# Kernel optimization log

Hardware: AMD Instinct MI355X
Metric: run time of the kernel (lower is better)

Reference implementation:

```python
import jax, jax.numpy as jnp
import numpy as np

N_ATOMS = 10000
N_STRUCT = 100
N_PSEUDO = 4
N_SPECIES = 4
NMAX = 8
LMAX = 3
HIDDEN = 256
Q = NMAX * N_PSEUDO            # 32 radial*pseudo channels per l
N_FEAT = (LMAX + 1) * Q * Q    # 4096


def setup_inputs() -> dict:
    key = jax.random.key(0)
    ks = jax.random.split(key, 12)
    inp = {}
    for l in range(LMAX + 1):
        inp[f"c{l}"] = jax.random.normal(ks[l], (N_ATOMS, 2 * l + 1, Q), dtype=jnp.float32)
    inp["species_idx"] = jax.random.randint(ks[4], (N_ATOMS,), 0, N_SPECIES, dtype=jnp.int32)
    inp["structure_ids"] = jnp.sort(jax.random.randint(ks[5], (N_ATOMS,), 0, N_STRUCT, dtype=jnp.int32))
    inp["comb_W"] = jax.random.normal(ks[6], (N_PSEUDO, N_SPECIES), dtype=jnp.float32) / np.sqrt(N_SPECIES).astype(np.float32)
    inp["W0"] = jax.random.normal(ks[7], (N_PSEUDO, N_FEAT, HIDDEN), dtype=jnp.float32) / np.sqrt(N_FEAT).astype(np.float32)
    inp["W1"] = jax.random.normal(ks[8], (N_PSEUDO, HIDDEN, HIDDEN), dtype=jnp.float32) / np.sqrt(HIDDEN).astype(np.float32)
    inp["W2"] = jax.random.normal(ks[9], (N_PSEUDO, HIDDEN, 1), dtype=jnp.float32) / np.sqrt(HIDDEN).astype(np.float32)
    return inp


def _power_spectrum(cs):
    # Per-atom outer-product contraction over m, per angular order l.
    feats = []
    for l, c in enumerate(cs):  # c: [A, 2l+1, Q]
        cg = np.float32(1.0 / np.sqrt(2 * l + 1))
        ps = cg * jnp.einsum('amq,amr->aqr', c, c)  # [A, Q, Q]
        feats.append(ps.reshape(c.shape[0], -1))
    return jnp.concatenate(feats, axis=-1)  # [A, N_FEAT]


def reference(c0, c1, c2, c3, species_idx, structure_ids, comb_W, W0, W1, W2):
    features = _power_spectrum([c0, c1, c2, c3])  # [A, F]
    # species-gathered pseudo-species weights: one_hot(a_i) @ combination_matrix
    one_hot = jax.nn.one_hot(species_idx, N_SPECIES, dtype=features.dtype)  # [A, S]
    pw = one_hot @ comb_W.T  # [A, P]
    # embedded_features = features[:, :, None] * pw[:, None, :]
    emb = features[:, None, :] * pw[:, :, None]  # [A, P, F]
    # distinct no-bias MLP per pseudo species (SiLU activations)
    h = jax.nn.silu(jnp.einsum('apf,pfh->aph', emb, W0))
    h = jax.nn.silu(jnp.einsum('aph,phg->apg', h, W1))
    atomic = jnp.einsum('apg,pgo->apo', h, W2)[..., 0].sum(axis=1)  # [A]
    # scatter-sum atomic energies into per-structure totals (index_add_)
    energies = jax.ops.segment_sum(atomic, structure_ids, num_segments=N_STRUCT)
    return energies.reshape(-1, 1)
```

## Files before the change

### kernel.cpp

```cpp
#include <hip/hip_runtime.h>
#include <hip/hip_bf16.h>
#include <cstdint>
#include <cstddef>

#define N_ATOMS 10000
#define NSTRUCT 100
#define NP 4
#define NS 4
#define NF2 2560
#define HID 256
#define APAD 10240

#define PB_FEAT  2500
#define PB_W0    (PB_FEAT + 2560)
#define PB_W1    (PB_W0 + 256)
#define PB_ZERO  (PB_W1 + 300)
#define PB_TOTAL (PB_ZERO + 1)

typedef __attribute__((ext_vector_type(8))) _Float16 f16x8;
typedef __attribute__((ext_vector_type(8))) ushort u16x8;
typedef __attribute__((ext_vector_type(4))) float f32x4;

__device__ __forceinline__ float silu(float x) {
  return x / (1.f + __expf(-x));
}
__device__ __forceinline__ ushort f2h(float x) {
  _Float16 h = (_Float16)x;
  return *reinterpret_cast<ushort*>(&h);
}
__device__ __forceinline__ void cdec(int c, int& q, int& b) {
  if (c < 32)      { q = c >> 2; b = c & 3; }
  else if (c < 56) { int x = c - 32; int j = (x * 171) >> 9; q = 8 + j; b = 1 + (x - j * 3); }
  else if (c < 72) { int x = c - 56; q = 16 + (x >> 1); b = 2 + (x & 1); }
  else             { q = 24 + (c - 72); b = 3; }
}

typedef __attribute__((address_space(3))) uint32_t lds_u32;
typedef const __attribute__((address_space(1))) uint32_t glb_u32;
__device__ __forceinline__ void glds16(const ushort* g, ushort* l) {
  __builtin_amdgcn_global_load_lds((glb_u32*)g, (lds_u32*)l, 16, 0, 0);
}

__global__ __launch_bounds__(256) void prep_kernel(
    const float* __restrict__ c0, const float* __restrict__ c1,
    const float* __restrict__ c2, const float* __restrict__ c3,
    const float* __restrict__ W0, const float* __restrict__ W1,
    ushort* __restrict__ fh, ushort* __restrict__ W0t,
    ushort* __restrict__ W1t, float* __restrict__ out) {
  __shared__ float shbuf[2048];
  int b = blockIdx.x;
  int tid = threadIdx.x;

  if (b < PB_FEAT) {
    int wv = tid >> 6, lane = tid & 63;
    int a = b * 4 + wv;
    float* cs = shbuf + wv * 512;
    for (int i = 0; i < 8; ++i) {
      int e = lane + i * 64;
      float v;
      if (e < 32)       v = c0[a * 32  + e];
      else if (e < 128) v = c1[a * 96  + (e - 32)];
      else if (e < 288) v = c2[a * 160 + (e - 128)];
      else              v = c3[a * 224 + (e - 288)];
      cs[e] = v;
    }
    __syncthreads();
    const float cg[4]  = {1.0f, 0.5773502691896258f, 0.4472135954999579f, 0.3779644730092272f};
    const int  off[4]  = {0, 32, 128, 288};
    const int  nm[4]   = {1, 3, 5, 7};
#pragma unroll
    for (int t = 0; t < 5; ++t) {
      int cc = lane + t * 64;
      int l = cc / 80, c = cc - l * 80;
      int q, bb; cdec(c, q, bb);
      int rb = bb * 8;
      const float* base = cs + off[l];
      float s[8] = {0.f, 0.f, 0.f, 0.f, 0.f, 0.f, 0.f, 0.f};
      for (int m = 0; m < nm[l]; ++m) {
        float bq = base[m * 32 + q];
        float4 v0 = *reinterpret_cast<const float4*>(&base[m * 32 + rb]);
        float4 v1 = *reinterpret_cast<const float4*>(&base[m * 32 + rb + 4]);
        s[0] += bq * v0.x; s[1] += bq * v0.y; s[2] += bq * v0.z; s[3] += bq * v0.w;
        s[4] += bq * v1.x; s[5] += bq * v1.y; s[6] += bq * v1.z; s[7] += bq * v1.w;
      }
      u16x8 o;
#pragma unroll
      for (int u = 0; u < 8; ++u) o[u] = f2h(s[u] * cg[l]);
      *reinterpret_cast<u16x8*>(&fh[(size_t)a * NF2 + cc * 8]) = o;
    }
  } else if (b < PB_W0) {
    int idx = b - PB_FEAT;
    int nx = idx & 7;
    int rest = idx >> 3;
    int ky = rest % 80, p = rest / 80;
    int kt = ky * 32, nt = nx * 32;
    int lx = tid & 31, ly = tid >> 5;
    float (*t)[33] = (float(*)[33])shbuf;
    const float* src = W0 + (size_t)p * 4096 * HID;
#pragma unroll
    for (int i = 0; i < 4; ++i) {
      int kf = kt + ly + i * 8;
      int l = kf / 640, w = kf - l * 640;
      int c = w >> 3, s = w & 7;
      int q, bb; cdec(c, q, bb);
      int r = bb * 8 + s;
      float v = 0.f;
      if (r >= q) {
        v = src[(size_t)(l * 1024 + q * 32 + r) * HID + nt + lx];
        if (r > q) v += src[(size_t)(l * 1024 + r * 32 + q) * HID + nt + lx];
      }
      t[ly + i * 8][lx] = v;
    }
    __syncthreads();
    ushort* dst = W0t + (size_t)p * HID * NF2;
#pragma unroll
    for (int i = 0; i < 4; ++i)
      dst[(size_t)(nt + ly + i * 8) * NF2 + kt + lx] = f2h(t[lx][ly + i * 8]);
  } else if (b < PB_W1) {
    int idx = b - PB_W0;
    int nx = idx & 7, ky = (idx >> 3) & 7, p = idx >> 6;
    int kt = ky * 32, nt = nx * 32;
    int lx = tid & 31, ly = tid >> 5;
    float (*t)[33] = (float(*)[33])shbuf;
    const float* src = W1 + (size_t)p * HID * HID;
#pragma unroll
    for (int i = 0; i < 4; ++i)
      t[ly + i * 8][lx] = src[(size_t)(kt + ly + i * 8) * HID + nt + lx];
    __syncthreads();
    ushort* dst = W1t + (size_t)p * HID * HID;
#pragma unroll
    for (int i = 0; i < 4; ++i)
      dst[(size_t)(nt + ly + i * 8) * HID + kt + lx] = f2h(t[lx][ly + i * 8]);
  } else if (b < PB_ZERO) {
    int idx = b - PB_W1;
    size_t e = (size_t)idx * 2048 + tid * 8;
    u16x8 z = (u16x8){0, 0, 0, 0, 0, 0, 0, 0};
    *reinterpret_cast<u16x8*>(&fh[(size_t)N_ATOMS * NF2 + e]) = z;
  } else {
    if (tid < NSTRUCT) out[tid] = 0.f;
  }
}

__global__ __launch_bounds__(256) void gemm0_mfma(
    const ushort* __restrict__ fh, const ushort* __restrict__ W0t,
    const float* __restrict__ combW, const int* __restrict__ species,
    ushort* __restrict__ h0f) {
  __shared__ ushort As[64 * 64];
  __shared__ ushort Bs[64 * 64];
  int tid = threadIdx.x;
  int linear = blockIdx.y * 8 + blockIdx.x;
  int xc = linear & 7, sq = linear >> 3;
  int bm = ((sq >> 3) * 8 + xc) * 128;
  int bn = (sq & 7) * 128;
  int wid = tid >> 6, lane = tid & 63;
  int wm = (wid >> 1) * 64, wn = (wid & 1) * 64;
  int mh = wid >> 1, nh = wid & 1;

  int pr = tid >> 3, pc = tid & 7;
  int lg = pc ^ (pr & 7);
  int mhalf = lg >> 2, kc = lg & 3;
  const ushort* gaA1 = fh  + ((size_t)(bm + pr + 64 * mhalf) * NF2 + kc * 8);
  const ushort* gaA2 = gaA1 + (size_t)32 * NF2;
  const ushort* gaB1 = W0t + ((size_t)(bn + pr + 64 * mhalf) * NF2 + kc * 8);
  const ushort* gaB2 = gaB1 + (size_t)32 * NF2;
  ushort* lA = As + tid * 8;
  ushort* lB = Bs + tid * 8;

  f32x4 acc[4][4];
#pragma unroll
  for (int i = 0; i < 4; ++i)
#pragma unroll
    for (int j = 0; j < 4; ++j) acc[i][j] = (f32x4){0.f, 0.f, 0.f, 0.f};

  int mrow = lane & 15;
  int h7 = mrow & 7;
  int qv = lane >> 4;
  int pcA = ((mh << 2) | qv) ^ h7;
  int pcB = ((nh << 2) | qv) ^ h7;

  for (int k0 = 0; k0 < NF2; k0 += 32) {
    glds16(gaA1 + k0, lA);
    glds16(gaA2 + k0, lA + 2048);
    glds16(gaB1 + k0, lB);
    glds16(gaB2 + k0, lB + 2048);
    __syncthreads();

    f16x8 af[4], bf[4];
#pragma unroll
    for (int i = 0; i < 4; ++i) {
      af[i] = *reinterpret_cast<const f16x8*>(&As[(i * 16 + mrow) * 64 + pcA * 8]);
      bf[i] = *reinterpret_cast<const f16x8*>(&Bs[(i * 16 + mrow) * 64 + pcB * 8]);
    }
#pragma unroll
    for (int i = 0; i < 4; ++i)
#pragma unroll
      for (int j = 0; j < 4; ++j)
        acc[i][j] = __builtin_amdgcn_mfma_f32_16x16x32_f16(af[i], bf[j], acc[i][j], 0, 0, 0);
    __syncthreads();
  }

  int p = bn >> 8;
  int col = lane & 15, rbase = (lane >> 4) * 4;
#pragma unroll
  for (int i = 0; i < 4; ++i) {
#pragma unroll
    for (int r = 0; r < 4; ++r) {
      int m = bm + wm + i * 16 + rbase + r;
      bool live = (m < N_ATOMS);
      float pw = live ? combW[p * NS + species[m]] : 0.f;
#pragma unroll
      for (int j = 0; j < 4; ++j) {
        int n = bn + wn + j * 16 + col;
        float v = live ? silu(pw * acc[i][j][r]) : 0.f;
        h0f[(size_t)m * 1024 + n] = f2h(v);
      }
    }
  }
}

__global__ __launch_bounds__(256) void mlp1_mfma(
    const ushort* __restrict__ h0f, const ushort* __restrict__ W1t,
    const float* __restrict__ W2, const int* __restrict__ sid,
    float* __restrict__ out) {
  __shared__ ushort As[64 * 256];
  __shared__ float sout[NSTRUCT];
  int tid = threadIdx.x;
  int linear = blockIdx.x;
  int xc = linear & 7, s = linear >> 3;
  int p = s & 3, t = s >> 2;
  int bm = ((t >> 1) * 8 + xc) * 128 + (t & 1) * 64;
  int wid = tid >> 6, lane = tid & 63;
  int wn = wid * 64;

  if (tid < NSTRUCT) sout[tid] = 0.f;

  int mrow = lane & 15;
  int qv = lane >> 4;
  int h7 = mrow & 7;

#pragma unroll
  for (int s8 = 0; s8 < 8; ++s8) {
    int d = s8 * 256 + tid;
    int r = d >> 5, pcs = d & 31;
    int lc = pcs ^ (r & 7);
    glds16(h0f + (size_t)(bm + r) * 1024 + p * 256 + lc * 8, As + d * 8);
  }

  const ushort* wb = W1t + (size_t)p * HID * HID;
  f16x8 breg[4][8];
#pragma unroll
  for (int j = 0; j < 4; ++j) {
    const ushort* row = wb + (size_t)(wn + j * 16 + mrow) * 256 + qv * 8;
#pragma unroll
    for (int ki = 0; ki < 8; ++ki)
      breg[j][ki] = *reinterpret_cast<const f16x8*>(row + ki * 32);
  }

  __syncthreads();

  f32x4 acc[4][4];
#pragma unroll
  for (int i = 0; i < 4; ++i)
#pragma unroll
    for (int j = 0; j < 4; ++j) acc[i][j] = (f32x4){0.f, 0.f, 0.f, 0.f};

#pragma unroll
  for (int ki = 0; ki < 8; ++ki) {
    f16x8 af[4];
#pragma unroll
    for (int i = 0; i < 4; ++i) {
      int row = i * 16 + mrow;
      int pc2 = (ki * 4 + qv) ^ h7;
      af[i] = *reinterpret_cast<const f16x8*>(&As[row * 256 + pc2 * 8]);
    }
#pragma unroll
    for (int i = 0; i < 4; ++i)
#pragma unroll
      for (int j = 0; j < 4; ++j)
        acc[i][j] = __builtin_amdgcn_mfma_f32_16x16x32_f16(af[i], breg[j][ki], acc[i][j], 0, 0, 0);
  }

  int col = lane & 15, quad = lane >> 4;
  float w2j[4];
#pragma unroll
  for (int j = 0; j < 4; ++j) w2j[j] = W2[p * 256 + wn + j * 16 + col];
#pragma unroll
  for (int i = 0; i < 4; ++i) {
#pragma unroll
    for (int r = 0; r < 4; ++r) {
      float v = silu(acc[i][0][r]) * w2j[0] + silu(acc[i][1][r]) * w2j[1]
              + silu(acc[i][2][r]) * w2j[2] + silu(acc[i][3][r]) * w2j[3];
      v += __shfl_xor(v, 1, 64);
      v += __shfl_xor(v, 2, 64);
      v += __shfl_xor(v, 4, 64);
      v += __shfl_xor(v, 8, 64);
      if (col == 0) {
        int m = bm + i * 16 + quad * 4 + r;
        if (m < N_ATOMS) atomicAdd(&sout[sid[m]], v);
      }
    }
  }
  __syncthreads();
  if (tid < NSTRUCT) {
    float v = sout[tid];
    if (v != 0.f) atomicAdd(&out[tid], v);
  }
}

extern "C" void kernel_launch(void* const* d_in, const int* in_sizes, int n_in,
                              void* d_out, int out_size, void* d_ws, size_t ws_size,
                              hipStream_t stream) {
  const float* c0      = (const float*)d_in[0];
  const float* c1      = (const float*)d_in[1];
  const float* c2      = (const float*)d_in[2];
  const float* c3      = (const float*)d_in[3];
  const int*   species = (const int*)d_in[4];
  const int*   sid     = (const int*)d_in[5];
  const float* combW   = (const float*)d_in[6];
  const float* W0      = (const float*)d_in[7];
  const float* W1      = (const float*)d_in[8];
  const float* W2      = (const float*)d_in[9];
  float*       out     = (float*)d_out;

  ushort* fh  = (ushort*)d_ws;
  ushort* W0t = fh  + (size_t)APAD * NF2;
  ushort* W1t = W0t + (size_t)NP * HID * NF2;
  ushort* h0f = W1t + (size_t)NP * HID * HID;

  prep_kernel<<<PB_TOTAL, 256, 0, stream>>>(c0, c1, c2, c3, W0, W1,
                                            fh, W0t, W1t, out);

  dim3 g2(8, APAD / 128);
  gemm0_mfma<<<g2, 256, 0, stream>>>(fh, W0t, combW, species, h0f);

  mlp1_mfma<<<640, 256, 0, stream>>>(h0f, W1t, W2, sid, out);
}
```

Measured before the change: 206.3 us.

## Fuse first-layer GEMM with second-layer MLP to eliminate h0 round trip

Merges the W0 GEMM kernel and the W1/W2 MLP kernel into one kernel. Each block computes a 64-row by 256-hidden tile for one pseudo species, writes the SiLU output into shared memory, then runs the W1 GEMM and W2 reduction from there. This removes the global write and read of the fp16 h0 buffer and one kernel launch. In exchange the first GEMM now uses 64x256 tiles with 4x more B traffic per A row, and W1 fragments are loaded inside the k loop rather than preloaded into registers.

```diff
diff --git a/kernel.cpp b/kernel.cpp
--- a/kernel.cpp
+++ b/kernel.cpp
@@ -141,89 +141,15 @@
   }
 }
 
-__global__ __launch_bounds__(256) void gemm0_mfma(
+__global__ __launch_bounds__(256) void gemm_fused(
     const ushort* __restrict__ fh, const ushort* __restrict__ W0t,
+    const ushort* __restrict__ W1t, const float* __restrict__ W2,
     const float* __restrict__ combW, const int* __restrict__ species,
-    ushort* __restrict__ h0f) {
-  __shared__ ushort As[64 * 64];
-  __shared__ ushort Bs[64 * 64];
-  int tid = threadIdx.x;
-  int linear = blockIdx.y * 8 + blockIdx.x;
-  int xc = linear & 7, sq = linear >> 3;
-  int bm = ((sq >> 3) * 8 + xc) * 128;
-  int bn = (sq & 7) * 128;
-  int wid = tid >> 6, lane = tid & 63;
-  int wm = (wid >> 1) * 64, wn = (wid & 1) * 64;
-  int mh = wid >> 1, nh = wid & 1;
-
-  int pr = tid >> 3, pc = tid & 7;
-  int lg = pc ^ (pr & 7);
-  int mhalf = lg >> 2, kc = lg & 3;
-  const ushort* gaA1 = fh  + ((size_t)(bm + pr + 64 * mhalf) * NF2 + kc * 8);
-  const ushort* gaA2 = gaA1 + (size_t)32 * NF2;
-  const ushort* gaB1 = W0t + ((size_t)(bn + pr + 64 * mhalf) * NF2 + kc * 8);
-  const ushort* gaB2 = gaB1 + (size_t)32 * NF2;
-  ushort* lA = As + tid * 8;
-  ushort* lB = Bs + tid * 8;
-
-  f32x4 acc[4][4];
-#pragma unroll
-  for (int i = 0; i < 4; ++i)
-#pragma unroll
-    for (int j = 0; j < 4; ++j) acc[i][j] = (f32x4){0.f, 0.f, 0.f, 0.f};
-
-  int mrow = lane & 15;
-  int h7 = mrow & 7;
-  int qv = lane >> 4;
-  int pcA = ((mh << 2) | qv) ^ h7;
-  int pcB = ((nh << 2) | qv) ^ h7;
-
-  for (int k0 = 0; k0 < NF2; k0 += 32) {
-    glds16(gaA1 + k0, lA);
-    glds16(gaA2 + k0, lA + 2048);
-    glds16(gaB1 + k0, lB);
-    glds16(gaB2 + k0, lB + 2048);
-    __syncthreads();
-
-    f16x8 af[4], bf[4];
-#pragma unroll
-    for (int i = 0; i < 4; ++i) {
-      af[i] = *reinterpret_cast<const f16x8*>(&As[(i * 16 + mrow) * 64 + pcA * 8]);
-      bf[i] = *reinterpret_cast<const f16x8*>(&Bs[(i * 16 + mrow) * 64 + pcB * 8]);
-    }
-#pragma unroll
-    for (int i = 0; i < 4; ++i)
-#pragma unroll
-      for (int j = 0; j < 4; ++j)
-        acc[i][j] = __builtin_amdgcn_mfma_f32_16x16x32_f16(af[i], bf[j], acc[i][j], 0, 0, 0);
-    __syncthreads();
-  }
-
-  int p = bn >> 8;
-  int col = lane & 15, rbase = (lane >> 4) * 4;
-#pragma unroll
-  for (int i = 0; i < 4; ++i) {
-#pragma unroll
-    for (int r = 0; r < 4; ++r) {
-      int m = bm + wm + i * 16 + rbase + r;
-      bool live = (m < N_ATOMS);
-      float pw = live ? combW[p * NS + species[m]] : 0.f;
-#pragma unroll
-      for (int j = 0; j < 4; ++j) {
-        int n = bn + wn + j * 16 + col;
-        float v = live ? silu(pw * acc[i][j][r]) : 0.f;
-        h0f[(size_t)m * 1024 + n] = f2h(v);
-      }
-    }
-  }
-}
-
-__global__ __launch_bounds__(256) void mlp1_mfma(
-    const ushort* __restrict__ h0f, const ushort* __restrict__ W1t,
-    const float* __restrict__ W2, const int* __restrict__ sid,
-    float* __restrict__ out) {
-  __shared__ ushort As[64 * 256];
+    const int* __restrict__ sid, float* __restrict__ out) {
+  __shared__ ushort smem[64 * 256];
   __shared__ float sout[NSTRUCT];
+  ushort* As = smem;
+  ushort* Bs = smem + 2048;
   int tid = threadIdx.x;
   int linear = blockIdx.x;
   int xc = linear & 7, s = linear >> 3;
@@ -234,53 +160,101 @@
 
   if (tid < NSTRUCT) sout[tid] = 0.f;
 
+  int prA = tid >> 3, pcA0 = tid & 7;
+  int lgA = pcA0 ^ (prA & 7);
+  const ushort* gaA = fh + ((size_t)(bm + prA + 32 * (lgA >> 2)) * NF2 + (lgA & 3) * 8);
+  ushort* lA = As + tid * 8;
+  int lgB = pcA0 ^ ((tid >> 3) & 7);
+  int nB = (tid >> 3) + 128 * (lgB >> 2);
+  const ushort* gaB = W0t + ((size_t)(p * 256 + nB) * NF2 + (lgB & 3) * 8);
+  ushort* lB = Bs + tid * 8;
+
+  f32x4 acc[4][4];
+#pragma unroll
+  for (int i = 0; i < 4; ++i)
+#pragma unroll
+    for (int j = 0; j < 4; ++j) acc[i][j] = (f32x4){0.f, 0.f, 0.f, 0.f};
+
   int mrow = lane & 15;
   int qv = lane >> 4;
   int h7 = mrow & 7;
 
-#pragma unroll
-  for (int s8 = 0; s8 < 8; ++s8) {
-    int d = s8 * 256 + tid;
-    int r = d >> 5, pcs = d & 31;
-    int lc = pcs ^ (r & 7);
-    glds16(h0f + (size_t)(bm + r) * 1024 + p * 256 + lc * 8, As + d * 8);
-  }
+  for (int k0 = 0; k0 < NF2; k0 += 32) {
+    glds16(gaA + k0, lA);
+#pragma unroll
+    for (int t3 = 0; t3 < 4; ++t3)
+      glds16(gaB + k0 + (size_t)t3 * 32 * NF2, lB + t3 * 2048);
+    __syncthreads();
+
+    f16x8 af[4], bf[4];
+#pragma unroll
+    for (int i = 0; i < 4; ++i) {
+      int m = i * 16 + mrow;
+      int pc = (((m >> 5) << 2) | qv) ^ (m & 7);
+      af[i] = *reinterpret_cast<const f16x8*>(&As[(m & 31) * 64 + pc * 8]);
+    }
+#pragma unroll
+    for (int j = 0; j < 4; ++j) {
+      int n = wn + j * 16 + mrow;
+      int pc = (((n >> 7) << 2) | qv) ^ (n & 7);
+      bf[j] = *reinterpret_cast<const f16x8*>(&Bs[(n & 127) * 64 + pc * 8]);
+    }
+#pragma unroll
+    for (int i = 0; i < 4; ++i)
+#pragma unroll
+      for (int j = 0; j < 4; ++j)
+        acc[i][j] = __builtin_amdgcn_mfma_f32_16x16x32_f16(af[i], bf[j], acc[i][j], 0, 0, 0);
+    __syncthreads();
+  }
+
+  int col = lane & 15, quad = lane >> 4;
+#pragma unroll
+  for (int i = 0; i < 4; ++i) {
+#pragma unroll
+    for (int r = 0; r < 4; ++r) {
+      int lm = i * 16 + quad * 4 + r;
+      int gm = bm + lm;
+      bool live = (gm < N_ATOMS);
+      float pw = live ? combW[p * NS + species[gm]] : 0.f;
+#pragma unroll
+      for (int j = 0; j < 4; ++j) {
+        int lh = wn + j * 16 + col;
+        float v = live ? silu(pw * acc[i][j][r]) : 0.f;
+        int pc2 = ((lh >> 3) ^ (lm & 7));
+        smem[lm * 256 + pc2 * 8 + (lh & 7)] = f2h(v);
+      }
+    }
+  }
+  __syncthreads();
+
+  f32x4 acc2[4][4];
+#pragma unroll
+  for (int i = 0; i < 4; ++i)
+#pragma unroll
+    for (int j = 0; j < 4; ++j) acc2[i][j] = (f32x4){0.f, 0.f, 0.f, 0.f};
 
   const ushort* wb = W1t + (size_t)p * HID * HID;
-  f16x8 breg[4][8];
-#pragma unroll
-  for (int j = 0; j < 4; ++j) {
-    const ushort* row = wb + (size_t)(wn + j * 16 + mrow) * 256 + qv * 8;
-#pragma unroll
-    for (int ki = 0; ki < 8; ++ki)
-      breg[j][ki] = *reinterpret_cast<const f16x8*>(row + ki * 32);
-  }
-
-  __syncthreads();
-
-  f32x4 acc[4][4];
-#pragma unroll
-  for (int i = 0; i < 4; ++i)
-#pragma unroll
-    for (int j = 0; j < 4; ++j) acc[i][j] = (f32x4){0.f, 0.f, 0.f, 0.f};
-
 #pragma unroll
   for (int ki = 0; ki < 8; ++ki) {
-    f16x8 af[4];
+    f16x8 bj[4];
+#pragma unroll
+    for (int j = 0; j < 4; ++j)
+      bj[j] = *reinterpret_cast<const f16x8*>(
+          wb + (size_t)(wn + j * 16 + mrow) * 256 + ki * 32 + qv * 8);
+    f16x8 af2[4];
 #pragma unroll
     for (int i = 0; i < 4; ++i) {
-      int row = i * 16 + mrow;
-      int pc2 = (ki * 4 + qv) ^ h7;
-      af[i] = *reinterpret_cast<const f16x8*>(&As[row * 256 + pc2 * 8]);
+      int lm = i * 16 + mrow;
+      int pc2 = (ki * 4 + qv) ^ (lm & 7);
+      af2[i] = *reinterpret_cast<const f16x8*>(&smem[lm * 256 + pc2 * 8]);
     }
 #pragma unroll
     for (int i = 0; i < 4; ++i)
 #pragma unroll
       for (int j = 0; j < 4; ++j)
-        acc[i][j] = __builtin_amdgcn_mfma_f32_16x16x32_f16(af[i], breg[j][ki], acc[i][j], 0, 0, 0);
-  }
-
-  int col = lane & 15, quad = lane >> 4;
+        acc2[i][j] = __builtin_amdgcn_mfma_f32_16x16x32_f16(af2[i], bj[j], acc2[i][j], 0, 0, 0);
+  }
+
   float w2j[4];
 #pragma unroll
   for (int j = 0; j < 4; ++j) w2j[j] = W2[p * 256 + wn + j * 16 + col];
@@ -288,8 +262,8 @@
   for (int i = 0; i < 4; ++i) {
 #pragma unroll
     for (int r = 0; r < 4; ++r) {
-      float v = silu(acc[i][0][r]) * w2j[0] + silu(acc[i][1][r]) * w2j[1]
-              + silu(acc[i][2][r]) * w2j[2] + silu(acc[i][3][r]) * w2j[3];
+      float v = silu(acc2[i][0][r]) * w2j[0] + silu(acc2[i][1][r]) * w2j[1]
+              + silu(acc2[i][2][r]) * w2j[2] + silu(acc2[i][3][r]) * w2j[3];
       v += __shfl_xor(v, 1, 64);
       v += __shfl_xor(v, 2, 64);
       v += __shfl_xor(v, 4, 64);
@@ -325,13 +299,10 @@
   ushort* fh  = (ushort*)d_ws;
   ushort* W0t = fh  + (size_t)APAD * NF2;
   ushort* W1t = W0t + (size_t)NP * HID * NF2;
-  ushort* h0f = W1t + (size_t)NP * HID * HID;
 
   prep_kernel<<<PB_TOTAL, 256, 0, stream>>>(c0, c1, c2, c3, W0, W1,
                                             fh, W0t, W1t, out);
 
-  dim3 g2(8, APAD / 128);
-  gemm0_mfma<<<g2, 256, 0, stream>>>(fh, W0t, combW, species, h0f);
-
-  mlp1_mfma<<<640, 256, 0, stream>>>(h0f, W1t, W2, sid, out);
-}
+  gemm_fused<<<640, 256, 0, stream>>>(fh, W0t, W1t, W2, combW, species,
+                                      sid, out);
+}
```

After: 247.4 us. +19.9%, slower.
